# Kernel optimization log

Hardware: AMD Instinct MI355X
Metric: run time of the kernel (lower is better)

## Reference

```python
import jax, jax.numpy as jnp
import numpy as np

B, R, A, L, P = 1024, 512, 196, 2, 4  # batch, rnn_size, att_size, num_layers, num_parallels


def setup_inputs() -> dict:
    key = jax.random.key(0)
    ks = jax.random.split(key, 24)
    s = 0.02
    inp = {
        'x': jax.random.normal(ks[0], (B, R), jnp.float32),
        'att': jax.random.normal(ks[1], (B, A, R), jnp.float32),
        'inputs': jax.random.normal(ks[2], (2 * L, B, R), jnp.float32),
        # first attention block
        'Wa2a': jax.random.normal(ks[3], (A, R), jnp.float32) * s,
        'ba2a': jnp.zeros((A,), jnp.float32),
        'Wh2a': jax.random.normal(ks[4], (A, R), jnp.float32) * s,
        'bh2a': jnp.zeros((A,), jnp.float32),
        'Wd2d': jax.random.normal(ks[5], (1, A), jnp.float32) * s,
        'bd2d': jnp.zeros((1,), jnp.float32),
        # second attention block
        'Wa2a1': jax.random.normal(ks[6], (A, R), jnp.float32) * s,
        'ba2a1': jnp.zeros((A,), jnp.float32),
        'Wh2a1': jax.random.normal(ks[7], (A, R), jnp.float32) * s,
        'bh2a1': jnp.zeros((A,), jnp.float32),
        'Wd2d1': jax.random.normal(ks[8], (1, A), jnp.float32) * s,
        'bd2d1': jnp.zeros((1,), jnp.float32),
        # per-parallel LSTM gate linears, stacked over P
        'Wi2h': jax.random.normal(ks[9], (P, 4 * R, R), jnp.float32) * s,
        'bi2h': jnp.zeros((P, 4 * R), jnp.float32),
        'Wh2h': jax.random.normal(ks[10], (P, 4 * R, R), jnp.float32) * s,
        'bh2h': jnp.zeros((P, 4 * R), jnp.float32),
        'Wa2h': jax.random.normal(ks[11], (P, 4 * R, R), jnp.float32) * s,
        'ba2h': jnp.zeros((P, 4 * R), jnp.float32),
    }
    return inp


def _attend(att, h, Wa, ba, Wh, bh, Wd, bd):
    # att: [B, S, R] with S == A (code requires it); h: [B, R]
    av = jnp.einsum('bsr,ar->bsa', att, Wa) + ba            # [B, S, A]
    ah = h @ Wh.T + bh                                      # [B, A]
    # original expands h-projection along the LAST axis (unsqueeze(2).expand)
    dot = jnp.tanh(av + ah[:, :, None])                     # [B, S, A]
    score = jnp.einsum('bsa,a->bs', dot, Wd[0]) + bd[0]     # [B, S]
    w = jax.nn.softmax(score, axis=-1)
    return jnp.einsum('bsr,bs->br', att, w)                 # [B, R]


def reference(x, att, inputs, Wa2a, ba2a, Wh2a, bh2a, Wd2d, bd2d,
              Wa2a1, ba2a1, Wh2a1, bh2a1, Wd2d1, bd2d1,
              Wi2h, bi2h, Wh2h, bh2h, Wa2h, ba2h):
    R_ = x.shape[-1]
    L_ = inputs.shape[0] // 2
    outputs = []
    for i in range(L_):
        prev_c = inputs[2 * i]
        prev_h = inputs[2 * i + 1]
        xt = x if i == 0 else x + outputs[-1]
        att_res = _attend(att, prev_h, Wa2a, ba2a, Wh2a, bh2a, Wd2d, bd2d)
        # stacked per-parallel gate sums: [P, B, 4R]
        sums = (jnp.einsum('bd,pgd->pbg', xt, Wi2h) + bi2h[:, None, :]
                + jnp.einsum('bd,pgd->pbg', prev_h, Wh2h) + bh2h[:, None, :]
                + jnp.einsum('bd,pgd->pbg', att_res, Wa2h) + ba2h[:, None, :])
        ig = jax.nn.sigmoid(sums[..., :R_])
        fg = jax.nn.sigmoid(sums[..., R_:2 * R_])
        og = jax.nn.sigmoid(sums[..., 2 * R_:3 * R_])
        it = jnp.tanh(sums[..., 3 * R_:])
        nc = fg * prev_c[None] + ig * it                    # [P, B, R]
        next_c = nc.mean(axis=0)
        next_h = (og * jnp.tanh(nc)).mean(axis=0)
        att_res1 = _attend(att, next_h, Wa2a1, ba2a1, Wh2a1, bh2a1, Wd2d1, bd2d1)
        top_h = att_res1 + next_h
        outputs.append(next_c)
        outputs.append(top_h)
    return jnp.stack(outputs)  # [2L, B, R]
```

## Files before the change

kernel.cpp:

```cpp
#include <hip/hip_runtime.h>
#include <math.h>

typedef __attribute__((ext_vector_type(8))) unsigned short ushort8_t;
typedef __attribute__((ext_vector_type(8))) short bf16x8;
typedef __attribute__((ext_vector_type(4))) float f32x4;

namespace {

constexpr int Bn = 1024;
constexpr int Rn = 512;
constexpr int An = 196;
constexpr int Gn = 8192;
constexpr int Kcat = 1536;
constexpr int NP = 224;
constexpr long ROWS = (long)Bn * An;

__device__ __forceinline__ float b2f(unsigned short u) {
  union { unsigned int i; float f; } v; v.i = ((unsigned int)u) << 16; return v.f;
}
__device__ __forceinline__ unsigned short f2b(float f) {
  union { float f; unsigned int i; } v; v.f = f;
  unsigned int r = v.i + 0x7fffu + ((v.i >> 16) & 1u);
  return (unsigned short)(r >> 16);
}
__device__ __forceinline__ float sigmf(float x) {
  return __builtin_amdgcn_rcpf(1.f + __expf(-x));
}
__device__ __forceinline__ float tanhf_fast(float x) {
  const float e = __expf(2.f * x);
  return 1.f - 2.f * __builtin_amdgcn_rcpf(e + 1.f);
}

__global__ __launch_bounds__(256)
void f2b_copy(const float* __restrict__ src, unsigned short* __restrict__ dst, long n)
{
  long i = ((long)blockIdx.x * 256 + threadIdx.x) * 8;
  const long stride = (long)gridDim.x * 256 * 8;
  for (; i + 8 <= n; i += stride) {
    float4 a = *(const float4*)(src + i);
    float4 b = *(const float4*)(src + i + 4);
    ushort8_t o;
    o[0] = f2b(a.x); o[1] = f2b(a.y); o[2] = f2b(a.z); o[3] = f2b(a.w);
    o[4] = f2b(b.x); o[5] = f2b(b.y); o[6] = f2b(b.z); o[7] = f2b(b.w);
    *(ushort8_t*)(dst + i) = o;
  }
}

__global__ __launch_bounds__(256)
void pack_wpad(const float* __restrict__ Wa0, const float* __restrict__ Wa1,
               unsigned short* __restrict__ Wp)
{
  long i = ((long)blockIdx.x * 256 + threadIdx.x) * 8;
  if (i >= 2L * NP * 512) return;
  const int set = (int)(i / (NP * 512));
  const int rem = (int)(i % (NP * 512));
  const int row = rem / 512, k = rem % 512;
  ushort8_t o;
  if (row < An) {
    const float* s = (set ? Wa1 : Wa0) + (long)row * 512 + k;
    float4 a = *(const float4*)s, b = *(const float4*)(s + 4);
    o[0] = f2b(a.x); o[1] = f2b(a.y); o[2] = f2b(a.z); o[3] = f2b(a.w);
    o[4] = f2b(b.x); o[5] = f2b(b.y); o[6] = f2b(b.z); o[7] = f2b(b.w);
  } else {
    o = ushort8_t{0,0,0,0,0,0,0,0};
  }
  *(ushort8_t*)(Wp + i) = o;
}

__global__ __launch_bounds__(256)
void pack_w(const float* __restrict__ Wi, const float* __restrict__ Wh,
            const float* __restrict__ Wa, unsigned short* __restrict__ W2)
{
  long i = ((long)blockIdx.x * 256 + threadIdx.x) * 8;
  if (i >= (long)Gn * Kcat) return;
  const int g = (int)(i / Kcat);
  const int k = (int)(i % Kcat);
  const float* src = (k < 512) ? Wi + (long)g * 512 + k
                   : (k < 1024) ? Wh + (long)g * 512 + (k - 512)
                   : Wa + (long)g * 512 + (k - 1024);
  float4 a = *(const float4*)src;
  float4 b = *(const float4*)(src + 4);
  ushort8_t o;
  o[0] = f2b(a.x); o[1] = f2b(a.y); o[2] = f2b(a.z); o[3] = f2b(a.w);
  o[4] = f2b(b.x); o[5] = f2b(b.y); o[6] = f2b(b.z); o[7] = f2b(b.w);
  *(ushort8_t*)(W2 + i) = o;
}

__global__ __launch_bounds__(256)
void pack_x(const float* __restrict__ xa, const float* __restrict__ xb,
            const float* __restrict__ h, const float* __restrict__ a,
            unsigned short* __restrict__ X2)
{
  long i = ((long)blockIdx.x * 256 + threadIdx.x) * 8;
  if (i >= (long)Bn * Kcat) return;
  const int b = (int)(i / Kcat);
  const int k = (int)(i % Kcat);
  ushort8_t o;
  if (k < 512) {
    const float* s = xa + (long)b * 512 + k;
    float4 v0 = *(const float4*)s, v1 = *(const float4*)(s + 4);
    if (xb) {
      const float* s2 = xb + (long)b * 512 + k;
      float4 w0 = *(const float4*)s2, w1 = *(const float4*)(s2 + 4);
      v0.x += w0.x; v0.y += w0.y; v0.z += w0.z; v0.w += w0.w;
      v1.x += w1.x; v1.y += w1.y; v1.z += w1.z; v1.w += w1.w;
    }
    o[0] = f2b(v0.x); o[1] = f2b(v0.y); o[2] = f2b(v0.z); o[3] = f2b(v0.w);
    o[4] = f2b(v1.x); o[5] = f2b(v1.y); o[6] = f2b(v1.z); o[7] = f2b(v1.w);
  } else {
    const float* s = (k < 1024) ? h + (long)b * 512 + (k - 512)
                                : a + (long)b * 512 + (k - 1024);
    float4 v0 = *(const float4*)s, v1 = *(const float4*)(s + 4);
    o[0] = f2b(v0.x); o[1] = f2b(v0.y); o[2] = f2b(v0.z); o[3] = f2b(v0.w);
    o[4] = f2b(v1.x); o[5] = f2b(v1.y); o[6] = f2b(v1.z); o[7] = f2b(v1.w);
  }
  *(ushort8_t*)(X2 + i) = o;
}

template<int MODE>
__global__ __launch_bounds__(256)
void av_fused(const unsigned short* __restrict__ A,
              const unsigned short* __restrict__ Wp,
              const float* __restrict__ bvec,
              const float* __restrict__ Wd,
              const float* __restrict__ ah0, const float* __restrict__ ah1,
              float* __restrict__ s0, float* __restrict__ s1,
              unsigned short* __restrict__ av_out)
{
  constexpr int LDP = 40;
  __shared__ unsigned short As[128 * LDP];
  __shared__ unsigned short Bs[NP * LDP];
  __shared__ float wds[NP], bas[NP];
  __shared__ float ahAs[128], ahBs[128];
  __shared__ float sbA[128], sbB[128];

  const int tid = threadIdx.x;
  const int lane = tid & 63, wid = tid >> 6;
  const int wr = wid >> 1, wc = wid & 1;
  const int fr = lane & 15, q = lane >> 4, kg = q * 8;
  const long row0 = (long)blockIdx.x * 128;

  if (tid < NP) {
    bas[tid] = (tid < An) ? bvec[tid] : 0.f;
    if (MODE == 0) wds[tid] = (tid < An) ? Wd[tid] : 0.f;
  }
  if (MODE == 0 && tid < 128) {
    ahAs[tid] = ah0[row0 + tid];
    ahBs[tid] = ah1[row0 + tid];
  }

  f32x4 acc[4][7] = {};

  const unsigned short* Ap = A + (row0 + (tid >> 1)) * 512 + (tid & 1) * 16;
  const unsigned short* Bp = Wp + (long)tid * 512;
  const bool bload = tid < NP;
  ushort8_t pa0 = *(const ushort8_t*)Ap;
  ushort8_t pa1 = *(const ushort8_t*)(Ap + 8);
  ushort8_t pb0{}, pb1{}, pb2{}, pb3{};
  if (bload) {
    pb0 = *(const ushort8_t*)(Bp);
    pb1 = *(const ushort8_t*)(Bp + 8);
    pb2 = *(const ushort8_t*)(Bp + 16);
    pb3 = *(const ushort8_t*)(Bp + 24);
  }
  const int swA = (tid >> 1) * LDP + (tid & 1) * 16;
  const int swB = tid * LDP;

  for (int kt = 0; kt < 512; kt += 32) {
    *(ushort8_t*)&As[swA] = pa0;
    *(ushort8_t*)&As[swA + 8] = pa1;
    if (bload) {
      *(ushort8_t*)&Bs[swB] = pb0;
      *(ushort8_t*)&Bs[swB + 8] = pb1;
      *(ushort8_t*)&Bs[swB + 16] = pb2;
      *(ushort8_t*)&Bs[swB + 24] = pb3;
    }
    if (kt + 32 < 512) {
      pa0 = *(const ushort8_t*)(Ap + kt + 32);
      pa1 = *(const ushort8_t*)(Ap + kt + 40);
      if (bload) {
        pb0 = *(const ushort8_t*)(Bp + kt + 32);
        pb1 = *(const ushort8_t*)(Bp + kt + 40);
        pb2 = *(const ushort8_t*)(Bp + kt + 48);
        pb3 = *(const ushort8_t*)(Bp + kt + 56);
      }
    }
    __syncthreads();
    bf16x8 af[4], bfr[7];
#pragma unroll
    for (int m = 0; m < 4; ++m)
      af[m] = *(const bf16x8*)&As[(wr * 64 + m * 16 + fr) * LDP + kg];
#pragma unroll
    for (int n = 0; n < 7; ++n)
      bfr[n] = *(const bf16x8*)&Bs[(wc * 112 + n * 16 + fr) * LDP + kg];
#pragma unroll
    for (int m = 0; m < 4; ++m)
#pragma unroll
      for (int n = 0; n < 7; ++n)
        acc[m][n] = __builtin_amdgcn_mfma_f32_16x16x32_bf16(af[m], bfr[n], acc[m][n], 0, 0, 0);
    __syncthreads();
  }

  if (MODE == 1) {
#pragma unroll
    for (int n = 0; n < 7; ++n) {
      const int col = wc * 112 + n * 16 + fr;
      if (col >= An) continue;
      const float bv = bas[col];
#pragma unroll
      for (int m = 0; m < 4; ++m) {
#pragma unroll
        for (int j = 0; j < 4; ++j) {
          const long row = row0 + wr * 64 + m * 16 + q * 4 + j;
          av_out[row * An + col] = f2b(acc[m][n][j] + bv);
        }
      }
    }
    return;
  }

  float pA[4][4], pB[4][4];
#pragma unroll
  for (int m = 0; m < 4; ++m)
#pragma unroll
    for (int j = 0; j < 4; ++j) { pA[m][j] = 0.f; pB[m][j] = 0.f; }

#pragma unroll
  for (int n = 0; n < 7; ++n) {
    const int col = wc * 112 + n * 16 + fr;
    const float wd = wds[col];
    const float bv = bas[col];
#pragma unroll
    for (int m = 0; m < 4; ++m) {
#pragma unroll
      for (int j = 0; j < 4; ++j) {
        const int rl = wr * 64 + m * 16 + q * 4 + j;
        const float av = acc[m][n][j] + bv;
        pA[m][j] += wd * tanhf_fast(av + ahAs[rl]);
        pB[m][j] += wd * tanhf_fast(av + ahBs[rl]);
      }
    }
  }
#pragma unroll
  for (int m = 0; m < 4; ++m)
#pragma unroll
    for (int j = 0; j < 4; ++j) {
#pragma unroll
      for (int off = 1; off < 16; off <<= 1) {
        pA[m][j] += __shfl_xor(pA[m][j], off);
        pB[m][j] += __shfl_xor(pB[m][j], off);
      }
    }
  __syncthreads();
  if (fr == 0 && wc == 0) {
#pragma unroll
    for (int m = 0; m < 4; ++m)
#pragma unroll
      for (int j = 0; j < 4; ++j) {
        const int rl = wr * 64 + m * 16 + q * 4 + j;
        sbA[rl] = pA[m][j]; sbB[rl] = pB[m][j];
      }
  }
  __syncthreads();
  if (fr == 0 && wc == 1) {
#pragma unroll
    for (int m = 0; m < 4; ++m)
#pragma unroll
      for (int j = 0; j < 4; ++j) {
        const int rl = wr * 64 + m * 16 + q * 4 + j;
        sbA[rl] += pA[m][j]; sbB[rl] += pB[m][j];
      }
  }
  __syncthreads();
  if (tid < 128) {
    s0[row0 + tid] = sbA[tid];
    s1[row0 + tid] = sbB[tid];
  }
}

__global__ __launch_bounds__(256)
void gemm_bf(const unsigned short* __restrict__ A, const unsigned short* __restrict__ Bm,
             const float* __restrict__ bias, float* __restrict__ C,
             int N, int K, int ldc)
{
  constexpr int LDP = 40;
  __shared__ unsigned short As[128 * LDP];
  __shared__ unsigned short Bs[128 * LDP];
  const int tid = threadIdx.x;
  const long row0 = (long)blockIdx.y * 128;
  const int col0 = blockIdx.x * 128;
  const int wid = tid >> 6, lane = tid & 63;
  const int wr = wid >> 1, wc = wid & 1;
  const int fr = lane & 15, kg = (lane >> 4) * 8;

  f32x4 acc[4][4] = {};

  const int srow = tid >> 1;
  const int skh = tid & 1;
  const unsigned short* Ap = A + (row0 + srow) * (long)K + skh * 16;
  const int bcol = col0 + srow;
  const unsigned short* Bp = Bm + (long)(bcol < N ? bcol : N - 1) * K + skh * 16;

  ushort8_t a0 = *(const ushort8_t*)(Ap);
  ushort8_t a1 = *(const ushort8_t*)(Ap + 8);
  ushort8_t b0 = *(const ushort8_t*)(Bp);
  ushort8_t b1 = *(const ushort8_t*)(Bp + 8);

  const int sw = srow * LDP + skh * 16;
  for (int kt = 0; kt < K; kt += 32) {
    *(ushort8_t*)&As[sw] = a0;
    *(ushort8_t*)&As[sw + 8] = a1;
    *(ushort8_t*)&Bs[sw] = b0;
    *(ushort8_t*)&Bs[sw + 8] = b1;
    if (kt + 32 < K) {
      a0 = *(const ushort8_t*)(Ap + kt + 32);
      a1 = *(const ushort8_t*)(Ap + kt + 40);
      b0 = *(const ushort8_t*)(Bp + kt + 32);
      b1 = *(const ushort8_t*)(Bp + kt + 40);
    }
    __syncthreads();
    bf16x8 af[4], bfr[4];
#pragma unroll
    for (int m = 0; m < 4; ++m)
      af[m] = *(const bf16x8*)&As[(wr * 64 + m * 16 + fr) * LDP + kg];
#pragma unroll
    for (int n = 0; n < 4; ++n)
      bfr[n] = *(const bf16x8*)&Bs[(wc * 64 + n * 16 + fr) * LDP + kg];
#pragma unroll
    for (int m = 0; m < 4; ++m)
#pragma unroll
      for (int n = 0; n < 4; ++n)
        acc[m][n] = __builtin_amdgcn_mfma_f32_16x16x32_bf16(af[m], bfr[n], acc[m][n], 0, 0, 0);
    __syncthreads();
  }

  const int crow = wr * 64 + (lane >> 4) * 4;
  const int ccol = wc * 64 + fr;
#pragma unroll
  for (int n = 0; n < 4; ++n) {
    const int col = col0 + ccol + n * 16;
    if (col >= N) continue;
    const float bv = bias ? bias[col] : 0.f;
#pragma unroll
    for (int m = 0; m < 4; ++m) {
      const long rb = row0 + crow + m * 16;
#pragma unroll
      for (int j = 0; j < 4; ++j)
        C[(rb + j) * (long)ldc + col] = acc[m][n][j] + bv;
    }
  }
}

__global__ __launch_bounds__(256)
void score1(const unsigned short* __restrict__ av, const float* __restrict__ ah,
            const float* __restrict__ Wd, float* __restrict__ s0)
{
  const int row = blockIdx.x * 4 + (threadIdx.x >> 6);
  const int lane = threadIdx.x & 63;
  const unsigned short* avp = av + (long)row * An;
  const float A0 = ah[row];
  float v0 = 0.f;
  for (int a = lane; a < An; a += 64)
    v0 += Wd[a] * tanhf_fast(b2f(avp[a]) + A0);
#pragma unroll
  for (int o = 32; o; o >>= 1) v0 += __shfl_down(v0, o);
  if (lane == 0) s0[row] = v0;
}

__global__ __launch_bounds__(256)
void softmax_rows(float* __restrict__ sc)
{
  const int b = blockIdx.x;
  const int t = threadIdx.x;
  float x = (t < An) ? sc[(long)b * An + t] : -3.0e38f;
  float m = x;
#pragma unroll
  for (int o = 32; o > 0; o >>= 1) m = fmaxf(m, __shfl_down(m, o));
  __shared__ float red[4];
  __shared__ float bmax, bsumv;
  const int wid = t >> 6;
  if ((t & 63) == 0) red[wid] = m;
  __syncthreads();
  if (t == 0) bmax = fmaxf(fmaxf(red[0], red[1]), fmaxf(red[2], red[3]));
  __syncthreads();
  float e = (t < An) ? __expf(x - bmax) : 0.f;
  float sm = e;
#pragma unroll
  for (int o = 32; o > 0; o >>= 1) sm += __shfl_down(sm, o);
  if ((t & 63) == 0) red[wid] = sm;
  __syncthreads();
  if (t == 0) bsumv = red[0] + red[1] + red[2] + red[3];
  __syncthreads();
  if (t < An) sc[(long)b * An + t] = e / bsumv;
}

template<bool DUAL>
__global__ __launch_bounds__(256)
void wsum2(const unsigned short* __restrict__ att,
           const float* __restrict__ w0, const float* __restrict__ w1,
           const float* __restrict__ add0,
           float* __restrict__ o0, float* __restrict__ o1)
{
  const int half = threadIdx.x >> 7;
  const int b = blockIdx.x * 2 + half;
  const int t = threadIdx.x & 127;
  __shared__ float ws0[2][An], ws1[2][An];
  for (int s = t; s < An; s += 128) {
    ws0[half][s] = w0[(long)b * An + s];
    if (DUAL) ws1[half][s] = w1[(long)b * An + s];
  }
  __syncthreads();
  const unsigned short* ap = att + (long)b * An * Rn + t * 4;
  float a00 = 0, a01 = 0, a02 = 0, a03 = 0;
  float a10 = 0, a11 = 0, a12 = 0, a13 = 0;
  for (int s = 0; s < An; ++s) {
    ushort4 u = *(const ushort4*)(ap + (long)s * Rn);
    const float f0 = b2f(u.x), f1 = b2f(u.y), f2 = b2f(u.z), f3 = b2f(u.w);
    const float v0 = ws0[half][s];
    a00 = fmaf(f0, v0, a00); a01 = fmaf(f1, v0, a01);
    a02 = fmaf(f2, v0, a02); a03 = fmaf(f3, v0, a03);
    if (DUAL) {
      const float v1 = ws1[half][s];
      a10 = fmaf(f0, v1, a10); a11 = fmaf(f1, v1, a11);
      a12 = fmaf(f2, v1, a12); a13 = fmaf(f3, v1, a13);
    }
  }
  const long base = (long)b * Rn + t * 4;
  if (add0) {
    float4 ad = *(const float4*)(add0 + base);
    a00 += ad.x; a01 += ad.y; a02 += ad.z; a03 += ad.w;
  }
  float4 r0 = make_float4(a00, a01, a02, a03);
  *(float4*)(o0 + base) = r0;
  if (DUAL) *(float4*)(o1 + base) = make_float4(a10, a11, a12, a13);
}

__global__ __launch_bounds__(256)
void gates_pw(const float* __restrict__ sums, const float* __restrict__ prev_c,
              float* __restrict__ out_c, float* __restrict__ nh,
              unsigned short* __restrict__ nh_bf)
{
  const int i = blockIdx.x * 256 + threadIdx.x;
  const int b = i >> 9;
  const int r = i & 511;
  const float c = prev_c[i];
  float aC = 0.f, aH = 0.f;
#pragma unroll
  for (int p = 0; p < 4; ++p) {
    const float* sp = sums + (long)b * Gn + p * 2048 + r;
    const float ig = sigmf(sp[0]);
    const float fg = sigmf(sp[512]);
    const float og = sigmf(sp[1024]);
    const float it = tanhf_fast(sp[1536]);
    const float nc = fmaf(fg, c, ig * it);
    aC += nc;
    aH = fmaf(og, tanhf_fast(nc), aH);
  }
  out_c[i] = aC * 0.25f;
  const float hv = aH * 0.25f;
  nh[i] = hv;
  nh_bf[i] = f2b(hv);
}

__global__ __launch_bounds__(256)
void bias3(const float* __restrict__ a, const float* __restrict__ b,
           const float* __restrict__ c, float* __restrict__ o, int n)
{
  const int i = blockIdx.x * 256 + threadIdx.x;
  if (i < n) o[i] = a[i] + b[i] + c[i];
}

}

extern "C" void kernel_launch(void* const* d_in, const int* in_sizes, int n_in,
                              void* d_out, int out_size, void* d_ws, size_t ws_size,
                              hipStream_t stream)
{
  const float* x      = (const float*)d_in[0];
  const float* att    = (const float*)d_in[1];
  const float* inputs = (const float*)d_in[2];
  const float* Wa2a   = (const float*)d_in[3];
  const float* ba2a   = (const float*)d_in[4];
  const float* Wh2a   = (const float*)d_in[5];
  const float* bh2a   = (const float*)d_in[6];
  const float* Wd2d   = (const float*)d_in[7];
  const float* Wa2a1  = (const float*)d_in[9];
  const float* ba2a1  = (const float*)d_in[10];
  const float* Wh2a1  = (const float*)d_in[11];
  const float* bh2a1  = (const float*)d_in[12];
  const float* Wd2d1  = (const float*)d_in[13];
  const float* Wi2h   = (const float*)d_in[15];
  const float* bi2h   = (const float*)d_in[16];
  const float* Wh2h   = (const float*)d_in[17];
  const float* bh2h   = (const float*)d_in[18];
  const float* Wa2h   = (const float*)d_in[19];
  const float* ba2h   = (const float*)d_in[20];
  (void)in_sizes; (void)n_in; (void)out_size; (void)ws_size;

  float* out = (float*)d_out;
  const float* prev_c0 = inputs + 0 * (long)Bn * Rn;
  const float* prev_h0 = inputs + 1 * (long)Bn * Rn;
  const float* prev_c1 = inputs + 2 * (long)Bn * Rn;
  const float* prev_h1 = inputs + 3 * (long)Bn * Rn;

  char* wsp = (char*)d_ws;
  size_t off = 0;
  auto alloc = [&](size_t bytes) -> void* {
    void* p = wsp + off;
    off += (bytes + 1023) & ~(size_t)1023;
    return p;
  };
  unsigned short* att_bf  = (unsigned short*)alloc(ROWS * Rn * 2);
  unsigned short* W2      = (unsigned short*)alloc((size_t)Gn * Kcat * 2);
  unsigned short* Wpad    = (unsigned short*)alloc((size_t)2 * NP * Rn * 2);
  unsigned short* wh2a_bf = (unsigned short*)alloc((size_t)An * Rn * 2);
  unsigned short* wh2a1_bf= (unsigned short*)alloc((size_t)An * Rn * 2);
  unsigned short* h0_bf   = (unsigned short*)alloc((size_t)Bn * Rn * 2);
  unsigned short* h1_bf   = (unsigned short*)alloc((size_t)Bn * Rn * 2);
  unsigned short* nh_bf   = (unsigned short*)alloc((size_t)Bn * Rn * 2);
  unsigned short* X2      = (unsigned short*)alloc((size_t)Bn * Kcat * 2);
  unsigned short* av1_bf  = (unsigned short*)alloc(ROWS * An * 2);
  float* ahA  = (float*)alloc(ROWS * 4);
  float* ahB  = (float*)alloc(ROWS * 4);
  float* ah1  = (float*)alloc(ROWS * 4);
  float* scA  = (float*)alloc(ROWS * 4);
  float* scB  = (float*)alloc(ROWS * 4);
  float* sc1  = (float*)alloc(ROWS * 4);
  float* res0 = (float*)alloc((size_t)Bn * Rn * 4);
  float* res1 = (float*)alloc((size_t)Bn * Rn * 4);
  float* nh   = (float*)alloc((size_t)Bn * Rn * 4);
  float* bsum = (float*)alloc((size_t)Gn * 4);
  float* sums = (float*)alloc((size_t)Bn * Gn * 4);

  const dim3 blk(256);
  unsigned short* Wpad0 = Wpad;
  unsigned short* Wpad1 = Wpad + (size_t)NP * Rn;

  f2b_copy<<<dim3(50176), blk, 0, stream>>>(att, att_bf, ROWS * Rn);
  pack_wpad<<<dim3(112), blk, 0, stream>>>(Wa2a, Wa2a1, Wpad);
  f2b_copy<<<dim3(49), blk, 0, stream>>>(Wh2a,  wh2a_bf,  (long)An * Rn);
  f2b_copy<<<dim3(49), blk, 0, stream>>>(Wh2a1, wh2a1_bf, (long)An * Rn);
  f2b_copy<<<dim3(256), blk, 0, stream>>>(prev_h0, h0_bf, (long)Bn * Rn);
  f2b_copy<<<dim3(256), blk, 0, stream>>>(prev_h1, h1_bf, (long)Bn * Rn);
  pack_w<<<dim3(6144), blk, 0, stream>>>(Wi2h, Wh2h, Wa2h, W2);
  bias3<<<dim3(Gn / 256), blk, 0, stream>>>(bi2h, bh2h, ba2h, bsum, Gn);

  gemm_bf<<<dim3(2, Bn / 128), blk, 0, stream>>>(h0_bf, wh2a_bf, bh2a, ahA, An, Rn, An);
  gemm_bf<<<dim3(2, Bn / 128), blk, 0, stream>>>(h1_bf, wh2a_bf, bh2a, ahB, An, Rn, An);

  av_fused<0><<<dim3(ROWS / 128), blk, 0, stream>>>(
      att_bf, Wpad0, ba2a, Wd2d, ahA, ahB, scA, scB, (unsigned short*)nullptr);
  softmax_rows<<<dim3(Bn), blk, 0, stream>>>(scA);
  softmax_rows<<<dim3(Bn), blk, 0, stream>>>(scB);
  wsum2<true><<<dim3(Bn / 2), blk, 0, stream>>>(att_bf, scA, scB, (const float*)nullptr, res0, res1);

  av_fused<1><<<dim3(ROWS / 128), blk, 0, stream>>>(
      att_bf, Wpad1, ba2a1, (const float*)nullptr, (const float*)nullptr,
      (const float*)nullptr, (float*)nullptr, (float*)nullptr, av1_bf);

  pack_x<<<dim3(768), blk, 0, stream>>>(x, (const float*)nullptr, prev_h0, res0, X2);
  gemm_bf<<<dim3(Gn / 128, Bn / 128), blk, 0, stream>>>(X2, W2, bsum, sums, Gn, Kcat, Gn);
  gates_pw<<<dim3(Bn * Rn / 256), blk, 0, stream>>>(sums, prev_c0, out + 0, nh, nh_bf);

  gemm_bf<<<dim3(2, Bn / 128), blk, 0, stream>>>(nh_bf, wh2a1_bf, bh2a1, ah1, An, Rn, An);
  score1<<<dim3((int)(ROWS / 4)), blk, 0, stream>>>(av1_bf, ah1, Wd2d1, sc1);
  softmax_rows<<<dim3(Bn), blk, 0, stream>>>(sc1);
  wsum2<false><<<dim3(Bn / 2), blk, 0, stream>>>(att_bf, sc1, (const float*)nullptr, nh,
                                                 out + (long)Bn * Rn, (float*)nullptr);

  pack_x<<<dim3(768), blk, 0, stream>>>(x, out + (long)Bn * Rn, prev_h1, res1, X2);
  gemm_bf<<<dim3(Gn / 128, Bn / 128), blk, 0, stream>>>(X2, W2, bsum, sums, Gn, Kcat, Gn);
  gates_pw<<<dim3(Bn * Rn / 256), blk, 0, stream>>>(sums, prev_c1, out + 2 * (long)Bn * Rn, nh, nh_bf);

  gemm_bf<<<dim3(2, Bn / 128), blk, 0, stream>>>(nh_bf, wh2a1_bf, bh2a1, ah1, An, Rn, An);
  score1<<<dim3((int)(ROWS / 4)), blk, 0, stream>>>(av1_bf, ah1, Wd2d1, sc1);
  softmax_rows<<<dim3(Bn), blk, 0, stream>>>(sc1);
  wsum2<false><<<dim3(Bn / 2), blk, 0, stream>>>(att_bf, sc1, (const float*)nullptr, nh,
                                                 out + 3 * (long)Bn * Rn, (float*)nullptr);
}
```

Measured before the change: 773.8 us.

## Fuse att bf16 conversion and both attention projections into one kernel

Replaces the separate fp32-to-bf16 att conversion and the two av_fused passes with a single 512-thread kernel. It reads att once in fp32, converts it in registers, writes the bf16 copy for later use, and computes both Wa2a and Wa2a1 projections against a concatenated 448-column weight tile. Waves 0-1 produce the first-block scores and waves 2-3 store the second-block av. This removes two full passes over the large att tensor. In exchange the kernel uses more LDS per block and more threads, which may reduce occupancy.

After: 737.4 us. 4.7% less time.

```diff
diff --git a/kernel.cpp b/kernel.cpp
--- a/kernel.cpp
+++ b/kernel.cpp
@@ -117,45 +117,49 @@
   *(ushort8_t*)(X2 + i) = o;
 }
 
-template<int MODE>
-__global__ __launch_bounds__(256)
-void av_fused(const unsigned short* __restrict__ A,
-              const unsigned short* __restrict__ Wp,
-              const float* __restrict__ bvec,
-              const float* __restrict__ Wd,
-              const float* __restrict__ ah0, const float* __restrict__ ah1,
-              float* __restrict__ s0, float* __restrict__ s1,
-              unsigned short* __restrict__ av_out)
+__global__ __launch_bounds__(512)
+void av_all(const float* __restrict__ A32,
+            unsigned short* __restrict__ att_out,
+            const unsigned short* __restrict__ Wcat,
+            const float* __restrict__ b0vec, const float* __restrict__ b1vec,
+            const float* __restrict__ Wd,
+            const float* __restrict__ ah0, const float* __restrict__ ah1,
+            float* __restrict__ s0, float* __restrict__ s1,
+            unsigned short* __restrict__ av_out)
 {
   constexpr int LDP = 40;
   __shared__ unsigned short As[128 * LDP];
-  __shared__ unsigned short Bs[NP * LDP];
-  __shared__ float wds[NP], bas[NP];
+  __shared__ unsigned short Bs[448 * LDP];
+  __shared__ float wds[NP], bas0[NP], bas1[NP];
   __shared__ float ahAs[128], ahBs[128];
   __shared__ float sbA[128], sbB[128];
 
   const int tid = threadIdx.x;
   const int lane = tid & 63, wid = tid >> 6;
-  const int wr = wid >> 1, wc = wid & 1;
+  const int wr = wid >> 2, wc = wid & 3;
   const int fr = lane & 15, q = lane >> 4, kg = q * 8;
   const long row0 = (long)blockIdx.x * 128;
 
   if (tid < NP) {
-    bas[tid] = (tid < An) ? bvec[tid] : 0.f;
-    if (MODE == 0) wds[tid] = (tid < An) ? Wd[tid] : 0.f;
-  }
-  if (MODE == 0 && tid < 128) {
-    ahAs[tid] = ah0[row0 + tid];
-    ahBs[tid] = ah1[row0 + tid];
+    bas0[tid] = (tid < An) ? b0vec[tid] : 0.f;
+    bas1[tid] = (tid < An) ? b1vec[tid] : 0.f;
+    wds[tid]  = (tid < An) ? Wd[tid] : 0.f;
+  }
+  if (tid >= 256 && tid < 384) {
+    ahAs[tid - 256] = ah0[row0 + tid - 256];
+    ahBs[tid - 256] = ah1[row0 + tid - 256];
   }
 
   f32x4 acc[4][7] = {};
 
-  const unsigned short* Ap = A + (row0 + (tid >> 1)) * 512 + (tid & 1) * 16;
-  const unsigned short* Bp = Wp + (long)tid * 512;
-  const bool bload = tid < NP;
-  ushort8_t pa0 = *(const ushort8_t*)Ap;
-  ushort8_t pa1 = *(const ushort8_t*)(Ap + 8);
+  const int arow = tid >> 2, akc = (tid & 3) * 8;
+  const float* Ap = A32 + (row0 + arow) * 512 + akc;
+  unsigned short* Aout = att_out + (row0 + arow) * 512 + akc;
+  const bool bload = tid < 448;
+  const unsigned short* Bp = Wcat + (long)tid * 512;
+
+  float4 fa0 = *(const float4*)Ap;
+  float4 fa1 = *(const float4*)(Ap + 4);
   ushort8_t pb0{}, pb1{}, pb2{}, pb3{};
   if (bload) {
     pb0 = *(const ushort8_t*)(Bp);
@@ -163,12 +167,15 @@
     pb2 = *(const ushort8_t*)(Bp + 16);
     pb3 = *(const ushort8_t*)(Bp + 24);
   }
-  const int swA = (tid >> 1) * LDP + (tid & 1) * 16;
+  const int swA = arow * LDP + akc;
   const int swB = tid * LDP;
 
   for (int kt = 0; kt < 512; kt += 32) {
-    *(ushort8_t*)&As[swA] = pa0;
-    *(ushort8_t*)&As[swA + 8] = pa1;
+    ushort8_t ua;
+    ua[0] = f2b(fa0.x); ua[1] = f2b(fa0.y); ua[2] = f2b(fa0.z); ua[3] = f2b(fa0.w);
+    ua[4] = f2b(fa1.x); ua[5] = f2b(fa1.y); ua[6] = f2b(fa1.z); ua[7] = f2b(fa1.w);
+    *(ushort8_t*)&As[swA] = ua;
+    *(ushort8_t*)(Aout + kt) = ua;
     if (bload) {
       *(ushort8_t*)&Bs[swB] = pb0;
       *(ushort8_t*)&Bs[swB + 8] = pb1;
@@ -176,8 +183,8 @@
       *(ushort8_t*)&Bs[swB + 24] = pb3;
     }
     if (kt + 32 < 512) {
-      pa0 = *(const ushort8_t*)(Ap + kt + 32);
-      pa1 = *(const ushort8_t*)(Ap + kt + 40);
+      fa0 = *(const float4*)(Ap + kt + 32);
+      fa1 = *(const float4*)(Ap + kt + 36);
       if (bload) {
         pb0 = *(const ushort8_t*)(Bp + kt + 32);
         pb1 = *(const ushort8_t*)(Bp + kt + 40);
@@ -201,58 +208,57 @@
     __syncthreads();
   }
 
-  if (MODE == 1) {
+  float pA[4][4], pB[4][4];
+#pragma unroll
+  for (int m = 0; m < 4; ++m)
+#pragma unroll
+    for (int j = 0; j < 4; ++j) { pA[m][j] = 0.f; pB[m][j] = 0.f; }
+
+  if (wc < 2) {
 #pragma unroll
     for (int n = 0; n < 7; ++n) {
       const int col = wc * 112 + n * 16 + fr;
-      if (col >= An) continue;
-      const float bv = bas[col];
+      const float wd = wds[col];
+      const float bv = bas0[col];
+#pragma unroll
+      for (int m = 0; m < 4; ++m) {
+#pragma unroll
+        for (int j = 0; j < 4; ++j) {
+          const int rl = wr * 64 + m * 16 + q * 4 + j;
+          const float av = acc[m][n][j] + bv;
+          pA[m][j] += wd * tanhf_fast(av + ahAs[rl]);
+          pB[m][j] += wd * tanhf_fast(av + ahBs[rl]);
+        }
+      }
+    }
+#pragma unroll
+    for (int m = 0; m < 4; ++m)
+#pragma unroll
+      for (int j = 0; j < 4; ++j) {
+#pragma unroll
+        for (int off = 1; off < 16; off <<= 1) {
+          pA[m][j] += __shfl_xor(pA[m][j], off);
+          pB[m][j] += __shfl_xor(pB[m][j], off);
+        }
+      }
+  } else {
+#pragma unroll
+    for (int n = 0; n < 7; ++n) {
+      const int col1 = (wc - 2) * 112 + n * 16 + fr;
+      if (col1 >= An) continue;
+      const float bv = bas1[col1];
 #pragma unroll
       for (int m = 0; m < 4; ++m) {
 #pragma unroll
         for (int j = 0; j < 4; ++j) {
           const long row = row0 + wr * 64 + m * 16 + q * 4 + j;
-          av_out[row * An + col] = f2b(acc[m][n][j] + bv);
+          av_out[row * An + col1] = f2b(acc[m][n][j] + bv);
         }
       }
     }
-    return;
-  }
-
-  float pA[4][4], pB[4][4];
-#pragma unroll
-  for (int m = 0; m < 4; ++m)
-#pragma unroll
-    for (int j = 0; j < 4; ++j) { pA[m][j] = 0.f; pB[m][j] = 0.f; }
-
-#pragma unroll
-  for (int n = 0; n < 7; ++n) {
-    const int col = wc * 112 + n * 16 + fr;
-    const float wd = wds[col];
-    const float bv = bas[col];
-#pragma unroll
-    for (int m = 0; m < 4; ++m) {
-#pragma unroll
-      for (int j = 0; j < 4; ++j) {
-        const int rl = wr * 64 + m * 16 + q * 4 + j;
-        const float av = acc[m][n][j] + bv;
-        pA[m][j] += wd * tanhf_fast(av + ahAs[rl]);
-        pB[m][j] += wd * tanhf_fast(av + ahBs[rl]);
-      }
-    }
-  }
-#pragma unroll
-  for (int m = 0; m < 4; ++m)
-#pragma unroll
-    for (int j = 0; j < 4; ++j) {
-#pragma unroll
-      for (int off = 1; off < 16; off <<= 1) {
-        pA[m][j] += __shfl_xor(pA[m][j], off);
-        pB[m][j] += __shfl_xor(pB[m][j], off);
-      }
-    }
-  __syncthreads();
-  if (fr == 0 && wc == 0) {
+  }
+  __syncthreads();
+  if (wc == 0 && fr == 0) {
 #pragma unroll
     for (int m = 0; m < 4; ++m)
 #pragma unroll
@@ -262,7 +268,7 @@
       }
   }
   __syncthreads();
-  if (fr == 0 && wc == 1) {
+  if (wc == 1 && fr == 0) {
 #pragma unroll
     for (int m = 0; m < 4; ++m)
 #pragma unroll
@@ -533,10 +539,7 @@
   float* sums = (float*)alloc((size_t)Bn * Gn * 4);
 
   const dim3 blk(256);
-  unsigned short* Wpad0 = Wpad;
-  unsigned short* Wpad1 = Wpad + (size_t)NP * Rn;
-
-  f2b_copy<<<dim3(50176), blk, 0, stream>>>(att, att_bf, ROWS * Rn);
+
   pack_wpad<<<dim3(112), blk, 0, stream>>>(Wa2a, Wa2a1, Wpad);
   f2b_copy<<<dim3(49), blk, 0, stream>>>(Wh2a,  wh2a_bf,  (long)An * Rn);
   f2b_copy<<<dim3(49), blk, 0, stream>>>(Wh2a1, wh2a1_bf, (long)An * Rn);
@@ -548,15 +551,11 @@
   gemm_bf<<<dim3(2, Bn / 128), blk, 0, stream>>>(h0_bf, wh2a_bf, bh2a, ahA, An, Rn, An);
   gemm_bf<<<dim3(2, Bn / 128), blk, 0, stream>>>(h1_bf, wh2a_bf, bh2a, ahB, An, Rn, An);
 
-  av_fused<0><<<dim3(ROWS / 128), blk, 0, stream>>>(
-      att_bf, Wpad0, ba2a, Wd2d, ahA, ahB, scA, scB, (unsigned short*)nullptr);
+  av_all<<<dim3((int)(ROWS / 128)), dim3(512), 0, stream>>>(
+      att, att_bf, Wpad, ba2a, ba2a1, Wd2d, ahA, ahB, scA, scB, av1_bf);
   softmax_rows<<<dim3(Bn), blk, 0, stream>>>(scA);
   softmax_rows<<<dim3(Bn), blk, 0, stream>>>(scB);
   wsum2<true><<<dim3(Bn / 2), blk, 0, stream>>>(att_bf, scA, scB, (const float*)nullptr, res0, res1);
-
-  av_fused<1><<<dim3(ROWS / 128), blk, 0, stream>>>(
-      att_bf, Wpad1, ba2a1, (const float*)nullptr, (const float*)nullptr,
-      (const float*)nullptr, (float*)nullptr, (float*)nullptr, av1_bf);
 
   pack_x<<<dim3(768), blk, 0, stream>>>(x, (const float*)nullptr, prev_h0, res0, X2);
   gemm_bf<<<dim3(Gn / 128, Bn / 128), blk, 0, stream>>>(X2, W2, bsum, sums, Gn, Kcat, Gn);
```
